# Optimization experiments

Hardware: AMD Instinct MI355X
Metric: run time of the kernel (lower is better)

The kernel has to match this reference:

```python
import jax, jax.numpy as jnp
import numpy as np

DIM = 1024
NUM_HEADS = 16
HEAD_DIM = DIM // NUM_HEADS
ROPE_THETA = 10000.0


def rms_norm(x, w):
    # torch nn.RMSNorm with eps=None uses finfo(dtype).eps
    eps = jnp.finfo(x.dtype).eps
    var = jnp.mean(jnp.square(x), axis=-1, keepdims=True)
    return x * jax.lax.rsqrt(var + eps) * w


def rope(x, pos, theta=ROPE_THETA):
    # x: (b, h, n, d), pos: (b, n) float positions. Rotate-half RoPE.
    d = x.shape[-1]
    inv_freq = theta ** (-jnp.arange(0, d, 2, dtype=x.dtype) / d)  # (d/2,)
    ang = pos[:, None, :, None] * inv_freq  # (b, 1, n, d/2)
    cos, sin = jnp.cos(ang), jnp.sin(ang)
    x1, x2 = jnp.split(x, 2, axis=-1)
    return jnp.concatenate([x1 * cos - x2 * sin, x1 * sin + x2 * cos], axis=-1)


def setup_inputs() -> dict:
    key = jax.random.key(0)
    ks = jax.random.split(key, 9)
    b, n = 2, 2048
    s = DIM ** -0.5
    return {
        "tgt": jax.random.normal(ks[0], (b, n, DIM), jnp.float32),
        "src": jax.random.normal(ks[1], (b, n, DIM), jnp.float32),
        "tgt_pos": jax.random.uniform(ks[2], (b, n), jnp.float32) * n,
        "src_pos": jax.random.uniform(ks[3], (b, n), jnp.float32) * n,
        "Wq": jax.random.normal(ks[4], (DIM, DIM), jnp.float32) * s,
        "Wkv": jax.random.normal(ks[5], (DIM, 2 * DIM), jnp.float32) * s,
        "Wo": jax.random.normal(ks[6], (DIM, DIM), jnp.float32) * s,
        "q_norm_w": jnp.ones((HEAD_DIM,), jnp.float32),
        "k_norm_w": jnp.ones((HEAD_DIM,), jnp.float32),
    }


def reference(tgt, src, tgt_pos, src_pos, Wq, Wkv, Wo, q_norm_w, k_norm_w):
    b, n, _ = tgt.shape
    m = src.shape[1]
    h, hd = NUM_HEADS, HEAD_DIM
    # q: (b, h, n, hd)
    q = (tgt @ Wq).reshape(b, n, h, hd).transpose(0, 2, 1, 3)
    # kv layout '(two h d)': split into k and v chunks first
    kv = (src @ Wkv).reshape(b, m, 2, h, hd)
    k = kv[:, :, 0].transpose(0, 2, 1, 3)  # (b, h, m, hd)
    v = kv[:, :, 1].transpose(0, 2, 1, 3)
    q = rms_norm(q, q_norm_w)
    k = rms_norm(k, k_norm_w)
    q = rope(q, tgt_pos)
    k = rope(k, src_pos)
    scores = jnp.einsum("bhnd,bhmd->bhnm", q, k) / (hd ** 0.5)
    attn = jax.nn.softmax(scores, axis=-1)
    x = jnp.einsum("bhnm,bhmd->bhnd", attn, v)
    x = x.transpose(0, 2, 1, 3).reshape(b, n, h * hd)
    return x @ Wo
```

## Files before the change

kernel.cpp:

```cpp
#include <hip/hip_runtime.h>
#include <hip/hip_bf16.h>
#include <stdint.h>

#define DIM 1024
#define NH 16
#define HD 64
#define BATCH 2
#define SEQ 2048
#define ROWS (BATCH*SEQ)
#define NS 2
#define CHUNK (SEQ/NS)
#define NT (CHUNK/64)

typedef __attribute__((ext_vector_type(8))) short bf16x8;
typedef __attribute__((ext_vector_type(4))) float f32x4;
typedef __attribute__((ext_vector_type(16))) float f32x16;
typedef __attribute__((ext_vector_type(4))) unsigned short u16x4;
typedef __attribute__((ext_vector_type(4))) unsigned int u32x4;

static __device__ __forceinline__ unsigned short f2bf(float f) {
    union { float f; uint32_t u; } v; v.f = f;
    uint32_t u = v.u;
    uint32_t rnd = 0x7fffu + ((u >> 16) & 1u);
    return (unsigned short)((u + rnd) >> 16);
}

static __device__ __forceinline__ unsigned cvt_pk_bf16(float lo, float hi) {
    unsigned r;
    asm("v_cvt_pk_bf16_f32 %0, %1, %2" : "=v"(r) : "v"(lo), "v"(hi));
    return r;
}

__global__ void k_conv2(const float* __restrict__ a, const float* __restrict__ b,
                        unsigned short* __restrict__ oa, unsigned short* __restrict__ ob) {
    int blk = blockIdx.x;
    const float* in = (blk < 4096) ? a : b;
    unsigned short* out = (blk < 4096) ? oa : ob;
    int i = ((blk & 4095) * 256 + threadIdx.x) * 4;
    f32x4 v = *(const f32x4*)(in + i);
    u16x4 o;
    o.x = f2bf(v.x); o.y = f2bf(v.y); o.z = f2bf(v.z); o.w = f2bf(v.w);
    *(u16x4*)(out + i) = o;
}

__global__ void k_transpose_all(const float* __restrict__ Wq, const float* __restrict__ Wkv,
                                const float* __restrict__ Wo,
                                unsigned short* __restrict__ WqT, unsigned short* __restrict__ WkvT,
                                unsigned short* __restrict__ WoT) {
    __shared__ float tile[32][33];
    int bx = blockIdx.x;
    const float* W; unsigned short* WT; int N, xb;
    if (bx < 32)      { W = Wq;  WT = WqT;  N = DIM;     xb = bx; }
    else if (bx < 96) { W = Wkv; WT = WkvT; N = 2 * DIM; xb = bx - 32; }
    else              { W = Wo;  WT = WoT;  N = DIM;     xb = bx - 96; }
    const int K = DIM;
    int nt = xb * 32, kt = blockIdx.y * 32;
    int x = threadIdx.x, y = threadIdx.y;
    #pragma unroll
    for (int i = 0; i < 32; i += 8)
        tile[y + i][x] = W[(size_t)(kt + y + i) * N + nt + x];
    __syncthreads();
    #pragma unroll
    for (int i = 0; i < 32; i += 8)
        WT[(size_t)(nt + y + i) * K + kt + x] = f2bf(tile[x][y + i]);
}

__launch_bounds__(256, 3)
__global__ void k_gemm_qkv(const unsigned short* __restrict__ tgt_b,
                           const unsigned short* __restrict__ src_b,
                           const unsigned short* __restrict__ WqT,
                           const unsigned short* __restrict__ WkvT,
                           const float* __restrict__ tpos, const float* __restrict__ spos,
                           const float* __restrict__ qw, const float* __restrict__ kw,
                           unsigned short* __restrict__ q_a, unsigned short* __restrict__ k_a,
                           unsigned short* __restrict__ v_t) {
    __shared__ __align__(16) unsigned short As[128 * 64];
    __shared__ __align__(16) unsigned short Bs[128 * 64];
    const int tid  = threadIdx.x;
    const int wid  = tid >> 6, lane = tid & 63;
    const int l15  = lane & 15, l4 = lane >> 4;
    const int bx = blockIdx.x;
    const unsigned short* A;  const unsigned short* BT;  int n0;
    if (bx < 8) { A = tgt_b; BT = WqT;  n0 = bx * 128; }
    else        { A = src_b; BT = WkvT; n0 = (bx - 8) * 128; }
    const int K = DIM;
    const int m0 = blockIdx.y * 128;
    const int wr = wid >> 1, wc = wid & 1;
    const int srow = lane >> 3, schunk = lane & 7;

    f32x4 acc[4][4] = {};

    for (int kt = 0; kt < K; kt += 64) {
        #pragma unroll
        for (int t = 0; t < 4; ++t) {
            int r  = (t * 4 + wid) * 8 + srow;
            int ck = schunk ^ (r & 7);
            const unsigned short* ga = A  + (size_t)(m0 + r) * K + kt + ck * 8;
            const unsigned short* gb = BT + (size_t)(n0 + r) * K + kt + ck * 8;
            unsigned short* la = As + (t * 4 + wid) * 512 + lane * 8;
            unsigned short* lb = Bs + (t * 4 + wid) * 512 + lane * 8;
            __builtin_amdgcn_global_load_lds((const __attribute__((address_space(1))) void*)ga,
                                             (__attribute__((address_space(3))) void*)la, 16, 0, 0);
            __builtin_amdgcn_global_load_lds((const __attribute__((address_space(1))) void*)gb,
                                             (__attribute__((address_space(3))) void*)lb, 16, 0, 0);
        }
        __syncthreads();
        #pragma unroll
        for (int k0 = 0; k0 < 2; ++k0) {
            bf16x8 af[4], bfr[4];
            int kk = k0 * 32 + l4 * 8;
            #pragma unroll
            for (int i = 0; i < 4; ++i) {
                int ar = wr * 64 + i * 16 + l15;
                af[i]  = *(const bf16x8*)((const char*)As + ar * 128 + ((kk * 2) ^ ((ar & 7) << 4)));
                int br = wc * 64 + i * 16 + l15;
                bfr[i] = *(const bf16x8*)((const char*)Bs + br * 128 + ((kk * 2) ^ ((br & 7) << 4)));
            }
            #pragma unroll
            for (int i = 0; i < 4; ++i)
                #pragma unroll
                for (int j = 0; j < 4; ++j)
                    acc[i][j] = __builtin_amdgcn_mfma_f32_16x16x32_bf16(af[i], bfr[j], acc[i][j], 0, 0, 0);
        }
        __syncthreads();
    }

    const int colbase = n0 + wc * 64;
    const int mode = (bx < 8) ? 0 : ((colbase < 1024) ? 1 : 2);

    if (mode == 2) {
        const int h = (colbase - 1024) >> 6;
        #pragma unroll
        for (int i = 0; i < 4; ++i)
            #pragma unroll
            for (int r = 0; r < 4; ++r) {
                int row = m0 + wr * 64 + i * 16 + l4 * 4 + r;
                int b = row >> 11, n = row & (SEQ - 1);
                unsigned short* dst = v_t + ((size_t)(b * NH + h) * 64) * SEQ + n;
                #pragma unroll
                for (int j = 0; j < 4; ++j)
                    dst[(size_t)(j * 16 + l15) * SEQ] = f2bf(acc[i][j][r]);
            }
        return;
    }

    const float* pos = (mode == 0) ? tpos : spos;
    const float* wt  = (mode == 0) ? qw : kw;
    unsigned short* outb = (mode == 0) ? q_a : k_a;
    const int h = colbase >> 6;
    const float QS = (mode == 0) ? 0.18033688011112042f : 1.0f;
    const float eps = 1.1920928955078125e-7f;

    float w4[4];
    #pragma unroll
    for (int j = 0; j < 4; ++j) w4[j] = wt[j * 16 + l15];
    float invf0 = __expf(-(float)(2 * l15) * (1.0f / 64.0f) * 9.21034037198f);
    float invf1 = __expf(-(float)(2 * (16 + l15)) * (1.0f / 64.0f) * 9.21034037198f);

    #pragma unroll
    for (int i = 0; i < 4; ++i)
        #pragma unroll
        for (int r = 0; r < 4; ++r) {
            int row = m0 + wr * 64 + i * 16 + l4 * 4 + r;
            float v0 = acc[i][0][r], v1 = acc[i][1][r], v2 = acc[i][2][r], v3 = acc[i][3][r];
            float ssq = v0 * v0 + v1 * v1 + v2 * v2 + v3 * v3;
            ssq += __shfl_xor(ssq, 1, 64);
            ssq += __shfl_xor(ssq, 2, 64);
            ssq += __shfl_xor(ssq, 4, 64);
            ssq += __shfl_xor(ssq, 8, 64);
            float sc = rsqrtf(ssq * (1.0f / 64.0f) + eps);
            v0 *= sc * w4[0]; v1 *= sc * w4[1]; v2 *= sc * w4[2]; v3 *= sc * w4[3];
            float p = pos[row];
            float s0, c0, s1, c1;
            sincosf(p * invf0, &s0, &c0);
            sincosf(p * invf1, &s1, &c1);
            float o0 = (v0 * c0 - v2 * s0) * QS;
            float o1 = (v1 * c1 - v3 * s1) * QS;
            float o2 = (v0 * s0 + v2 * c0) * QS;
            float o3 = (v1 * s1 + v3 * c1) * QS;
            int b = row >> 11, n = row & (SEQ - 1);
            unsigned short* dst = outb + ((size_t)(b * NH + h) * SEQ + n) * 64;
            dst[l15]      = f2bf(o0);
            dst[16 + l15] = f2bf(o1);
            dst[32 + l15] = f2bf(o2);
            dst[48 + l15] = f2bf(o3);
        }
}

__launch_bounds__(256)
__global__ void k_gemm_bt(const unsigned short* __restrict__ A,
                          const unsigned short* __restrict__ BT,
                          float* __restrict__ C, int M, int N, int K) {
    __shared__ __align__(16) unsigned short As[128 * 64];
    __shared__ __align__(16) unsigned short Bs[128 * 64];
    const int tid  = threadIdx.x;
    const int wid  = tid >> 6, lane = tid & 63;
    const int l15  = lane & 15, l4 = lane >> 4;
    const int m0 = blockIdx.y * 128, n0 = blockIdx.x * 128;
    const int wr = wid >> 1, wc = wid & 1;
    const int srow = lane >> 3, schunk = lane & 7;

    f32x4 acc[4][4] = {};

    for (int kt = 0; kt < K; kt += 64) {
        #pragma unroll
        for (int t = 0; t < 4; ++t) {
            int r  = (t * 4 + wid) * 8 + srow;
            int ck = schunk ^ (r & 7);
            const unsigned short* ga = A  + (size_t)(m0 + r) * K + kt + ck * 8;
            const unsigned short* gb = BT + (size_t)(n0 + r) * K + kt + ck * 8;
            unsigned short* la = As + (t * 4 + wid) * 512 + lane * 8;
            unsigned short* lb = Bs + (t * 4 + wid) * 512 + lane * 8;
            __builtin_amdgcn_global_load_lds((const __attribute__((address_space(1))) void*)ga,
                                             (__attribute__((address_space(3))) void*)la, 16, 0, 0);
            __builtin_amdgcn_global_load_lds((const __attribute__((address_space(1))) void*)gb,
                                             (__attribute__((address_space(3))) void*)lb, 16, 0, 0);
        }
        __syncthreads();
        #pragma unroll
        for (int k0 = 0; k0 < 2; ++k0) {
            bf16x8 af[4], bfr[4];
            int kk = k0 * 32 + l4 * 8;
            #pragma unroll
            for (int i = 0; i < 4; ++i) {
                int ar = wr * 64 + i * 16 + l15;
                af[i]  = *(const bf16x8*)((const char*)As + ar * 128 + ((kk * 2) ^ ((ar & 7) << 4)));
                int br = wc * 64 + i * 16 + l15;
                bfr[i] = *(const bf16x8*)((const char*)Bs + br * 128 + ((kk * 2) ^ ((br & 7) << 4)));
            }
            #pragma unroll
            for (int i = 0; i < 4; ++i)
                #pragma unroll
                for (int j = 0; j < 4; ++j)
                    acc[i][j] = __builtin_amdgcn_mfma_f32_16x16x32_bf16(af[i], bfr[j], acc[i][j], 0, 0, 0);
        }
        __syncthreads();
    }
    #pragma unroll
    for (int i = 0; i < 4; ++i) {
        int rb = m0 + wr * 64 + i * 16 + l4 * 4;
        #pragma unroll
        for (int j = 0; j < 4; ++j) {
            int col = n0 + wc * 64 + j * 16 + l15;
            #pragma unroll
            for (int r = 0; r < 4; ++r)
                C[(size_t)(rb + r) * N + col] = acc[i][j][r];
        }
    }
}

__launch_bounds__(256, 2)
__global__ void k_attn_part(const unsigned short* __restrict__ q_a,
                            const unsigned short* __restrict__ k_a,
                            const unsigned short* __restrict__ v_t,
                            float* __restrict__ o_part, float* __restrict__ ml) {
    __shared__ __align__(16) unsigned short K_lds[2][64 * 64];
    const int tid = threadIdx.x;
    const int wid = tid >> 6, lane = tid & 63;
    const int l31 = lane & 31, hi = lane >> 5;
    const int bh = blockIdx.z, ns = blockIdx.y;
    const int q0 = blockIdx.x * 256 + wid * 64;
    const unsigned short* qb = q_a + (size_t)bh * SEQ * 64;
    const unsigned short* kb = k_a + (size_t)bh * SEQ * 64;
    const unsigned short* vb = v_t + (size_t)bh * 64 * SEQ;
    const int kv_beg = ns * CHUNK;

    auto STAGE = [&](int buf, int kv0) {
        #pragma unroll
        for (int i = 0; i < 2; ++i) {
            int row = i * 32 + (tid >> 3);
            int ck = (tid & 7) ^ (row & 7);
            const unsigned short* gk = kb + (size_t)(kv0 + row) * 64 + ck * 8;
            __builtin_amdgcn_global_load_lds((const __attribute__((address_space(1))) void*)gk,
                (__attribute__((address_space(3))) void*)(&K_lds[buf][i * 2048 + tid * 8]), 16, 0, 0);
        }
    };

    STAGE(0, kv_beg);

    bf16x8 qfr[2][4];
    #pragma unroll
    for (int qf = 0; qf < 2; ++qf)
        #pragma unroll
        for (int c = 0; c < 4; ++c)
            qfr[qf][c] = *(const bf16x8*)(qb + (size_t)(q0 + qf * 32 + l31) * 64 + c * 16 + hi * 8);

    const unsigned short* vrow0 = vb + (size_t)l31 * SEQ;
    const unsigned short* vrow1 = vb + (size_t)(32 + l31) * SEQ;

    f32x16 oacc[2][2] = {};
    float lsum[2] = {0.f, 0.f};
    const int swz = (l31 & 7) << 4;

    __syncthreads();
    int buf = 0;
    for (int t = 0; t < NT; ++t) {
        if (t + 1 < NT) STAGE(buf ^ 1, kv_beg + (t + 1) * 64);
        const int kv0 = kv_beg + t * 64;
        f32x16 sacc[2][2] = {};
        #pragma unroll
        for (int ks = 0; ks < 2; ++ks) {
            const char* Kb = (const char*)K_lds[buf] + (ks * 32 + l31) * 128;
            #pragma unroll
            for (int c = 0; c < 4; ++c) {
                bf16x8 kf = *(const bf16x8*)(Kb + ((c * 32 + hi * 16) ^ swz));
                sacc[0][ks] = __builtin_amdgcn_mfma_f32_32x32x16_bf16(kf, qfr[0][c], sacc[0][ks], 0, 0, 0);
                sacc[1][ks] = __builtin_amdgcn_mfma_f32_32x32x16_bf16(kf, qfr[1][c], sacc[1][ks], 0, 0, 0);
            }
        }
        #pragma unroll
        for (int ks = 0; ks < 2; ++ks)
            #pragma unroll
            for (int kc = 0; kc < 2; ++kc) {
                bf16x8 vf[2];
                vf[0] = *(const bf16x8*)(vrow0 + kv0 + ks * 32 + kc * 16 + hi * 8);
                vf[1] = *(const bf16x8*)(vrow1 + kv0 + ks * 32 + kc * 16 + hi * 8);
                #pragma unroll
                for (int qf = 0; qf < 2; ++qf) {
                    float p[8];
                    #pragma unroll
                    for (int j = 0; j < 8; ++j)
                        p[j] = __builtin_amdgcn_exp2f(sacc[qf][ks][kc * 8 + j]);
                    lsum[qf] += ((p[0] + p[1]) + (p[2] + p[3])) + ((p[4] + p[5]) + (p[6] + p[7]));
                    unsigned a0 = cvt_pk_bf16(p[0], p[1]);
                    unsigned a1 = cvt_pk_bf16(p[2], p[3]);
                    unsigned b0 = cvt_pk_bf16(p[4], p[5]);
                    unsigned b1 = cvt_pk_bf16(p[6], p[7]);
                    asm("v_permlane32_swap_b32 %0, %1" : "+v"(a0), "+v"(b0));
                    asm("v_permlane32_swap_b32 %0, %1" : "+v"(a1), "+v"(b1));
                    u32x4 w; w.x = a0; w.y = a1; w.z = b0; w.w = b1;
                    bf16x8 pa = __builtin_bit_cast(bf16x8, w);
                    #pragma unroll
                    for (int dh = 0; dh < 2; ++dh)
                        oacc[qf][dh] = __builtin_amdgcn_mfma_f32_32x32x16_bf16(pa, vf[dh], oacc[qf][dh], 0, 0, 0);
                }
            }
        __syncthreads();
        buf ^= 1;
    }

    lsum[0] += __shfl_xor(lsum[0], 32, 64);
    lsum[1] += __shfl_xor(lsum[1], 32, 64);

    const size_t chunkbase = ((size_t)bh * NS + ns) * SEQ;
    #pragma unroll
    for (int qf = 0; qf < 2; ++qf) {
        #pragma unroll
        for (int r = 0; r < 16; ++r) {
            int qrow = (r & 3) + 8 * (r >> 2) + 4 * hi;
            size_t rowbase = (chunkbase + q0 + qf * 32 + qrow) * 64;
            o_part[rowbase + l31]      = oacc[qf][0][r];
            o_part[rowbase + 32 + l31] = oacc[qf][1][r];
        }
        if (hi == 0)
            ml[chunkbase + q0 + qf * 32 + l31] = lsum[qf];
    }
}

__launch_bounds__(256)
__global__ void k_combine(const float* __restrict__ o_part, const float* __restrict__ ml,
                          unsigned short* __restrict__ xo) {
    int wid = threadIdx.x >> 6, lane = threadIdx.x & 63;
    int idx = blockIdx.x * 4 + wid;
    int bh = idx >> 11, q = idx & (SEQ - 1);
    const size_t base = ((size_t)bh * NS) * SEQ + q;

    float O = 0.f, L = 0.f;
    #pragma unroll
    for (int i = 0; i < NS; ++i) {
        L += ml[base + (size_t)i * SEQ];
        O += o_part[(base + (size_t)i * SEQ) * 64 + lane];
    }
    int b = bh >> 4, h = bh & 15;
    xo[(size_t)(b * SEQ + q) * DIM + h * 64 + lane] = f2bf(O / L);
}

extern "C" void kernel_launch(void* const* d_in, const int* in_sizes, int n_in,
                              void* d_out, int out_size, void* d_ws, size_t ws_size,
                              hipStream_t stream) {
    const float* tgt  = (const float*)d_in[0];
    const float* src  = (const float*)d_in[1];
    const float* tpos = (const float*)d_in[2];
    const float* spos = (const float*)d_in[3];
    const float* Wq   = (const float*)d_in[4];
    const float* Wkv  = (const float*)d_in[5];
    const float* Wo   = (const float*)d_in[6];
    const float* qw   = (const float*)d_in[7];
    const float* kw   = (const float*)d_in[8];
    float* out = (float*)d_out;
    char* ws = (char*)d_ws;

    unsigned short* tgt_b = (unsigned short*)(ws);
    unsigned short* src_b = (unsigned short*)(ws + ( 8u << 20));
    unsigned short* WqT   = (unsigned short*)(ws + (16u << 20));
    unsigned short* WkvT  = (unsigned short*)(ws + (18u << 20));
    unsigned short* WoT   = (unsigned short*)(ws + (22u << 20));
    float*          o_prt = (float*)         (ws + (48u << 20));
    unsigned short* q_a   = (unsigned short*)(ws + (88u << 20));
    unsigned short* k_a   = (unsigned short*)(ws + (96u << 20));
    unsigned short* v_t   = (unsigned short*)(ws + (104u << 20));
    float*          ml    = (float*)         (ws + (112u << 20));
    unsigned short* x_b   = (unsigned short*)(ws);

    k_conv2<<<8192, 256, 0, stream>>>(tgt, src, tgt_b, src_b);
    k_transpose_all<<<dim3(128, 32), dim3(32, 8), 0, stream>>>(Wq, Wkv, Wo, WqT, WkvT, WoT);
    k_gemm_qkv<<<dim3(24, 32), 256, 0, stream>>>(tgt_b, src_b, WqT, WkvT,
                                                 tpos, spos, qw, kw, q_a, k_a, v_t);
    k_attn_part<<<dim3(SEQ / 256, NS, BATCH * NH), 256, 0, stream>>>(q_a, k_a, v_t, o_prt, ml);
    k_combine<<<BATCH * NH * SEQ / 4, 256, 0, stream>>>(o_prt, ml, x_b);
    k_gemm_bt<<<dim3( 8, 32), 256, 0, stream>>>(x_b, WoT, out, ROWS, DIM, DIM);
}
```

Before: 131.6 us.

## Store K and V in MFMA-fragment order and load directly from global memory

The QKV GEMM epilogue now writes K and V in a pre-swizzled layout that matches the per-lane MFMA operand order. The attention kernel can then load each 64-key tile with coalesced 16-byte loads straight into registers. This removes the LDS staging of K, the double buffering and the per-tile barriers. It gives up the async prefetch overlap, so global load latency is now exposed unless other waves hide it. The epilogue also writes more scattered 2-byte stores.

```diff
diff --git a/kernel.cpp b/kernel.cpp
--- a/kernel.cpp
+++ b/kernel.cpp
@@ -72,8 +72,8 @@
                            const unsigned short* __restrict__ WkvT,
                            const float* __restrict__ tpos, const float* __restrict__ spos,
                            const float* __restrict__ qw, const float* __restrict__ kw,
-                           unsigned short* __restrict__ q_a, unsigned short* __restrict__ k_a,
-                           unsigned short* __restrict__ v_t) {
+                           unsigned short* __restrict__ q_a, unsigned short* __restrict__ k_f,
+                           unsigned short* __restrict__ v_f) {
     __shared__ __align__(16) unsigned short As[128 * 64];
     __shared__ __align__(16) unsigned short Bs[128 * 64];
     const int tid  = threadIdx.x;
@@ -135,18 +135,23 @@
             #pragma unroll
             for (int r = 0; r < 4; ++r) {
                 int row = m0 + wr * 64 + i * 16 + l4 * 4 + r;
-                int b = row >> 11, n = row & (SEQ - 1);
-                unsigned short* dst = v_t + ((size_t)(b * NH + h) * 64) * SEQ + n;
+                int b = row >> 11, mm = row & (SEQ - 1);
+                int bh = b * NH + h;
+                int t = mm >> 6, ks = (mm >> 5) & 1, kc = (mm >> 4) & 1;
+                int hiv = (mm >> 3) & 1, e = mm & 7;
                 #pragma unroll
-                for (int j = 0; j < 4; ++j)
-                    dst[(size_t)(j * 16 + l15) * SEQ] = f2bf(acc[i][j][r]);
+                for (int j = 0; j < 4; ++j) {
+                    int dh = j >> 1, l31v = (j & 1) * 16 + l15;
+                    size_t idx = (((((size_t)(bh * 32 + t) * 2 + ks) * 2 + kc) * 2 + dh) * 2 + hiv) * 256
+                                 + l31v * 8 + e;
+                    v_f[idx] = f2bf(acc[i][j][r]);
+                }
             }
         return;
     }
 
     const float* pos = (mode == 0) ? tpos : spos;
     const float* wt  = (mode == 0) ? qw : kw;
-    unsigned short* outb = (mode == 0) ? q_a : k_a;
     const int h = colbase >> 6;
     const float QS = (mode == 0) ? 0.18033688011112042f : 1.0f;
     const float eps = 1.1920928955078125e-7f;
@@ -179,11 +184,22 @@
             float o2 = (v0 * s0 + v2 * c0) * QS;
             float o3 = (v1 * s1 + v3 * c1) * QS;
             int b = row >> 11, n = row & (SEQ - 1);
-            unsigned short* dst = outb + ((size_t)(b * NH + h) * SEQ + n) * 64;
-            dst[l15]      = f2bf(o0);
-            dst[16 + l15] = f2bf(o1);
-            dst[32 + l15] = f2bf(o2);
-            dst[48 + l15] = f2bf(o3);
+            if (mode == 0) {
+                unsigned short* dst = q_a + ((size_t)(b * NH + h) * SEQ + n) * 64;
+                dst[l15]      = f2bf(o0);
+                dst[16 + l15] = f2bf(o1);
+                dst[32 + l15] = f2bf(o2);
+                dst[48 + l15] = f2bf(o3);
+            } else {
+                int bh = b * NH + h;
+                int t = n >> 6, ksn = (n >> 5) & 1, l31k = n & 31;
+                int hik = l15 >> 3, e = l15 & 7;
+                size_t base = ((size_t)(bh * 32 + t) * 2 + ksn) * 4;
+                k_f[(base + 0) * 512 + hik * 256 + l31k * 8 + e] = f2bf(o0);
+                k_f[(base + 1) * 512 + hik * 256 + l31k * 8 + e] = f2bf(o1);
+                k_f[(base + 2) * 512 + hik * 256 + l31k * 8 + e] = f2bf(o2);
+                k_f[(base + 3) * 512 + hik * 256 + l31k * 8 + e] = f2bf(o3);
+            }
         }
 }
 
@@ -251,32 +267,15 @@
 
 __launch_bounds__(256, 2)
 __global__ void k_attn_part(const unsigned short* __restrict__ q_a,
-                            const unsigned short* __restrict__ k_a,
-                            const unsigned short* __restrict__ v_t,
+                            const unsigned short* __restrict__ k_f,
+                            const unsigned short* __restrict__ v_f,
                             float* __restrict__ o_part, float* __restrict__ ml) {
-    __shared__ __align__(16) unsigned short K_lds[2][64 * 64];
     const int tid = threadIdx.x;
     const int wid = tid >> 6, lane = tid & 63;
     const int l31 = lane & 31, hi = lane >> 5;
     const int bh = blockIdx.z, ns = blockIdx.y;
     const int q0 = blockIdx.x * 256 + wid * 64;
     const unsigned short* qb = q_a + (size_t)bh * SEQ * 64;
-    const unsigned short* kb = k_a + (size_t)bh * SEQ * 64;
-    const unsigned short* vb = v_t + (size_t)bh * 64 * SEQ;
-    const int kv_beg = ns * CHUNK;
-
-    auto STAGE = [&](int buf, int kv0) {
-        #pragma unroll
-        for (int i = 0; i < 2; ++i) {
-            int row = i * 32 + (tid >> 3);
-            int ck = (tid & 7) ^ (row & 7);
-            const unsigned short* gk = kb + (size_t)(kv0 + row) * 64 + ck * 8;
-            __builtin_amdgcn_global_load_lds((const __attribute__((address_space(1))) void*)gk,
-                (__attribute__((address_space(3))) void*)(&K_lds[buf][i * 2048 + tid * 8]), 16, 0, 0);
-        }
-    };
-
-    STAGE(0, kv_beg);
 
     bf16x8 qfr[2][4];
     #pragma unroll
@@ -285,36 +284,41 @@
         for (int c = 0; c < 4; ++c)
             qfr[qf][c] = *(const bf16x8*)(qb + (size_t)(q0 + qf * 32 + l31) * 64 + c * 16 + hi * 8);
 
-    const unsigned short* vrow0 = vb + (size_t)l31 * SEQ;
-    const unsigned short* vrow1 = vb + (size_t)(32 + l31) * SEQ;
+    const bf16x8* kf8 = (const bf16x8*)k_f;
+    const bf16x8* vf8 = (const bf16x8*)v_f;
 
     f32x16 oacc[2][2] = {};
     float lsum[2] = {0.f, 0.f};
-    const int swz = (l31 & 7) << 4;
-
-    __syncthreads();
-    int buf = 0;
+
     for (int t = 0; t < NT; ++t) {
-        if (t + 1 < NT) STAGE(buf ^ 1, kv_beg + (t + 1) * 64);
-        const int kv0 = kv_beg + t * 64;
+        const size_t tg = (size_t)bh * 32 + ns * NT + t;
+        const bf16x8* kt = kf8 + tg * 512;
+        const bf16x8* vt = vf8 + tg * 512;
+
+        bf16x8 kf[2][4];
+        #pragma unroll
+        for (int ks = 0; ks < 2; ++ks)
+            #pragma unroll
+            for (int c = 0; c < 4; ++c)
+                kf[ks][c] = kt[((ks * 4 + c) * 2 + hi) * 32 + l31];
+
         f32x16 sacc[2][2] = {};
         #pragma unroll
-        for (int ks = 0; ks < 2; ++ks) {
-            const char* Kb = (const char*)K_lds[buf] + (ks * 32 + l31) * 128;
+        for (int ks = 0; ks < 2; ++ks)
             #pragma unroll
             for (int c = 0; c < 4; ++c) {
-                bf16x8 kf = *(const bf16x8*)(Kb + ((c * 32 + hi * 16) ^ swz));
-                sacc[0][ks] = __builtin_amdgcn_mfma_f32_32x32x16_bf16(kf, qfr[0][c], sacc[0][ks], 0, 0, 0);
-                sacc[1][ks] = __builtin_amdgcn_mfma_f32_32x32x16_bf16(kf, qfr[1][c], sacc[1][ks], 0, 0, 0);
-            }
-        }
+                sacc[0][ks] = __builtin_amdgcn_mfma_f32_32x32x16_bf16(kf[ks][c], qfr[0][c], sacc[0][ks], 0, 0, 0);
+                sacc[1][ks] = __builtin_amdgcn_mfma_f32_32x32x16_bf16(kf[ks][c], qfr[1][c], sacc[1][ks], 0, 0, 0);
+            }
+
         #pragma unroll
         for (int ks = 0; ks < 2; ++ks)
             #pragma unroll
             for (int kc = 0; kc < 2; ++kc) {
                 bf16x8 vf[2];
-                vf[0] = *(const bf16x8*)(vrow0 + kv0 + ks * 32 + kc * 16 + hi * 8);
-                vf[1] = *(const bf16x8*)(vrow1 + kv0 + ks * 32 + kc * 16 + hi * 8);
+                #pragma unroll
+                for (int dh = 0; dh < 2; ++dh)
+                    vf[dh] = vt[(((ks * 2 + kc) * 2 + dh) * 2 + hi) * 32 + l31];
                 #pragma unroll
                 for (int qf = 0; qf < 2; ++qf) {
                     float p[8];
@@ -335,8 +339,6 @@
                         oacc[qf][dh] = __builtin_amdgcn_mfma_f32_32x32x16_bf16(pa, vf[dh], oacc[qf][dh], 0, 0, 0);
                 }
             }
-        __syncthreads();
-        buf ^= 1;
     }
 
     lsum[0] += __shfl_xor(lsum[0], 32, 64);
@@ -397,16 +399,16 @@
     unsigned short* WoT   = (unsigned short*)(ws + (22u << 20));
     float*          o_prt = (float*)         (ws + (48u << 20));
     unsigned short* q_a   = (unsigned short*)(ws + (88u << 20));
-    unsigned short* k_a   = (unsigned short*)(ws + (96u << 20));
-    unsigned short* v_t   = (unsigned short*)(ws + (104u << 20));
+    unsigned short* k_f   = (unsigned short*)(ws + (96u << 20));
+    unsigned short* v_f   = (unsigned short*)(ws + (104u << 20));
     float*          ml    = (float*)         (ws + (112u << 20));
     unsigned short* x_b   = (unsigned short*)(ws);
 
     k_conv2<<<8192, 256, 0, stream>>>(tgt, src, tgt_b, src_b);
     k_transpose_all<<<dim3(128, 32), dim3(32, 8), 0, stream>>>(Wq, Wkv, Wo, WqT, WkvT, WoT);
     k_gemm_qkv<<<dim3(24, 32), 256, 0, stream>>>(tgt_b, src_b, WqT, WkvT,
-                                                 tpos, spos, qw, kw, q_a, k_a, v_t);
-    k_attn_part<<<dim3(SEQ / 256, NS, BATCH * NH), 256, 0, stream>>>(q_a, k_a, v_t, o_prt, ml);
+                                                 tpos, spos, qw, kw, q_a, k_f, v_f);
+    k_attn_part<<<dim3(SEQ / 256, NS, BATCH * NH), 256, 0, stream>>>(q_a, k_f, v_f, o_prt, ml);
     k_combine<<<BATCH * NH * SEQ / 4, 256, 0, stream>>>(o_prt, ml, x_b);
     k_gemm_bt<<<dim3( 8, 32), 256, 0, stream>>>(x_b, WoT, out, ROWS, DIM, DIM);
 }
```

Measured after the change: 128.4 us. 2.4% less time.
